# Kernel tuning notes

Hardware: AMD Instinct MI355X
Metric: run time of the kernel (lower is better)

## Reference

```python
import jax, jax.numpy as jnp
from jax import lax
import numpy as np

OUT_CH = 16      # texture_features
INTER = 32       # texture_features_intermediate
TEXDIM = 1024    # texture_dimensions
IN_SIZE = 76


def _leaky(x):
    return jnp.where(x >= 0, x, 0.02 * x)


def grid_sample_bilinear_border(tex, grid):
    """torch.nn.functional.grid_sample, mode='bilinear', padding_mode='border',
    align_corners=False.  tex: (N,C,H,W); grid: (N,Ho,Wo,2) with (x,y) in [-1,1].
    N == 1 here; vectorized over H,W via fancy indexing."""
    N, C, H, W = tex.shape
    x, y = grid[..., 0], grid[..., 1]
    # unnormalize (align_corners=False)
    ix = ((x + 1.0) * W - 1.0) * 0.5
    iy = ((y + 1.0) * H - 1.0) * 0.5
    # border padding: clamp continuous coords
    ix = jnp.clip(ix, 0.0, W - 1.0)
    iy = jnp.clip(iy, 0.0, H - 1.0)
    x0 = jnp.floor(ix); y0 = jnp.floor(iy)
    wx = ix - x0; wy = iy - y0
    x0i = jnp.clip(x0, 0, W - 1).astype(jnp.int32)
    x1i = jnp.clip(x0 + 1, 0, W - 1).astype(jnp.int32)
    y0i = jnp.clip(y0, 0, H - 1).astype(jnp.int32)
    y1i = jnp.clip(y0 + 1, 0, H - 1).astype(jnp.int32)
    t = tex[0]  # (C,H,W)
    v00 = t[:, y0i[0], x0i[0]]  # (C,Ho,Wo)
    v01 = t[:, y0i[0], x1i[0]]
    v10 = t[:, y1i[0], x0i[0]]
    v11 = t[:, y1i[0], x1i[0]]
    wx = wx[0][None]; wy = wy[0][None]  # (1,Ho,Wo) broadcast over C
    out = (v00 * (1 - wx) * (1 - wy) + v01 * wx * (1 - wy)
           + v10 * (1 - wx) * wy + v11 * wx * wy)
    return out[None]  # (1,C,Ho,Wo)


def setup_inputs() -> dict:
    key = jax.random.key(0)
    ks = jax.random.split(key, 11)
    expressions = jax.random.normal(ks[0], (1, IN_SIZE), jnp.float32)
    audio_features = jax.random.normal(ks[1], (1, 16), jnp.float32)
    uv_inputs = jax.random.uniform(ks[2], (1, 2, 1024, 1024), jnp.float32, -1.0, 1.0)
    data = jax.random.normal(ks[3], (1, INTER, TEXDIM, TEXDIM), jnp.float32)
    def lin(kw, kb, fo, fi):
        s = 1.0 / np.sqrt(fi).astype(np.float32)
        return (jax.random.uniform(kw, (fo, fi), jnp.float32, -s, s),
                jax.random.uniform(kb, (fo,), jnp.float32, -s, s))
    W1, b1 = lin(ks[4], ks[5], 128, IN_SIZE)
    W2, b2 = lin(ks[6], ks[7], 64, 128)
    W3, b3 = lin(ks[8], ks[9], OUT_CH * 4 * 4 * INTER, 64)
    return {"expressions": expressions, "audio_features": audio_features,
            "uv_inputs": uv_inputs, "data": data,
            "W1": W1, "b1": b1, "W2": W2, "b2": b2, "W3": W3, "b3": b3}


def reference(expressions, audio_features, uv_inputs, data, W1, b1, W2, b2, W3, b3):
    # tiny MLP -> dynamic 4x4 conv filter
    h = expressions.reshape(1, 1, -1)
    h = _leaky(h @ W1.T + b1)
    h = _leaky(h @ W2.T + b2)
    f = jnp.tanh(h @ W3.T + b3)
    conv_filter = f.reshape(OUT_CH, INTER, 4, 4)
    # conv2d(data, filter, stride=1, padding=2) -> (1, OUT_CH, D+1, D+1)
    tex_eval = lax.conv_general_dilated(
        data, conv_filter, window_strides=(1, 1), padding=((2, 2), (2, 2)),
        dimension_numbers=("NCHW", "OIHW", "NCHW"))
    # grid: stack x (chan 0) and y (chan 1) along last dim
    grid = jnp.stack([uv_inputs[:, 0], uv_inputs[:, 1]], axis=3)  # (1,Ho,Wo,2)
    return grid_sample_bilinear_border(tex_eval, grid)
```

## Files before the change

### kernel.cpp

```cpp
#include <hip/hip_runtime.h>
#include <math.h>

#define NPX   1048576
#define TD    1025
#define PW    35
#define PH    11
#define DPAD  1028
#define ROWB  65792
#define DP_OFF 67289152

typedef _Float16 half8 __attribute__((ext_vector_type(8)));
typedef _Float16 half4 __attribute__((ext_vector_type(4)));
typedef float    f32x4 __attribute__((ext_vector_type(4)));

__device__ __forceinline__ void load_lds16(const void* g, void* lds) {
    __builtin_amdgcn_global_load_lds(
        (const __attribute__((address_space(1))) void*)g,
        (__attribute__((address_space(3))) void*)lds, 16, 0, 0);
}

__global__ __launch_bounds__(256) void mlp_kernel(
    const float* __restrict__ expr,
    const float* __restrict__ W1, const float* __restrict__ b1,
    const float* __restrict__ W2, const float* __restrict__ b2,
    const float* __restrict__ W3, const float* __restrict__ b3,
    _Float16* __restrict__ ffrag_g)
{
    __shared__ float sx[76];
    __shared__ float sh1[128];
    __shared__ float sh2[64];
    int t = threadIdx.x;
    if (t < 76) sx[t] = expr[t];
    __syncthreads();
    if (t < 128) {
        float a = b1[t];
        const float* w = W1 + t * 76;
        #pragma unroll 4
        for (int i = 0; i < 76; ++i) a += sx[i] * w[i];
        sh1[t] = a >= 0.f ? a : 0.02f * a;
    }
    __syncthreads();
    if (t < 64) {
        float a = b2[t];
        const float* w = W2 + t * 128;
        #pragma unroll 4
        for (int i = 0; i < 128; ++i) a += sh1[i] * w[i];
        sh2[t] = a >= 0.f ? a : 0.02f * a;
    }
    __syncthreads();
    int o = blockIdx.x * 256 + t;
    float a = b3[o];
    const float* w = W3 + o * 64;
    #pragma unroll 4
    for (int i = 0; i < 64; ++i) a += sh2[i] * w[i];
    a = tanhf(a);
    int oc = o >> 9;
    int ic = (o >> 4) & 31;
    int kk = o & 15;
    ffrag_g[(size_t)(kk * 64 + (ic >> 3) * 16 + oc) * 8 + (ic & 7)] = (_Float16)a;
}

__global__ __launch_bounds__(256) void repack_kernel(
    const float* __restrict__ data, _Float16* __restrict__ Dp)
{
    __shared__ _Float16 s[256 * 32];
    int tid = threadIdx.x;
    int Y = blockIdx.y;
    int X = blockIdx.x * 256 + tid;
    int y = Y - 2, x = X - 2;
    bool ok = ((unsigned)y < 1024u) && ((unsigned)x < 1024u);
    const float* dp = data + ((size_t)y << 10) + x;

    float v[32];
    #pragma unroll
    for (int j = 0; j < 32; ++j) v[j] = 0.f;
    if (ok) {
        #pragma unroll
        for (int j = 0; j < 32; ++j) v[j] = __builtin_nontemporal_load(&dp[(size_t)j * NPX]);
    }
    #pragma unroll
    for (int g = 0; g < 4; ++g) {
        half8 h;
        #pragma unroll
        for (int j = 0; j < 8; ++j) h[j] = (_Float16)v[g * 8 + j];
        int chunk = tid * 4 + g;
        int sw = chunk ^ ((chunk >> 3) & 7);
        *(half8*)((char*)s + sw * 16) = h;
    }
    __syncthreads();
    char* rowbase = (char*)Dp + (size_t)Y * ROWB + blockIdx.x * 16384;
    int lim = ROWB - blockIdx.x * 16384;
    #pragma unroll
    for (int i = 0; i < 4; ++i) {
        int off = tid * 16 + i * 4096;
        if (off < lim) {
            int chunk = tid + i * 256;
            int sw = chunk ^ ((chunk >> 3) & 7);
            *(uint4*)(rowbase + off) = *(uint4*)((char*)s + sw * 16);
        }
    }
}

__global__ __launch_bounds__(256, 6) void conv_mfma_kernel(
    const _Float16* __restrict__ Dp,
    const _Float16* __restrict__ ffrag_g,
    _Float16* __restrict__ tex)
{
    __shared__ __attribute__((aligned(128))) _Float16 sp[PH * PW * 32];

    int tid = threadIdx.x;
    int l = tid & 63, w = tid >> 6;
    int ox0 = blockIdx.x * 32;
    int oy0 = blockIdx.y * 8;

    half8 bfrag[16];
    #pragma unroll
    for (int kk = 0; kk < 16; ++kk)
        bfrag[kk] = *(const half8*)&ffrag_g[kk * 512 + l * 8];

    int lsw = l ^ ((l >> 3) & 7);
    for (int r = w; r < PH; r += 4) {
        int gy = min(oy0 + r, DPAD - 1);
        const char* grow = (const char*)Dp + (size_t)gy * ROWB;
        _Float16* lrow = sp + r * (PW * 32);
        #pragma unroll
        for (int c = 0; c < 3; ++c) {
            int off = ox0 * 64 + c * 1024 + lsw * 16;
            off = min(off, ROWB - 16);
            if (c < 2 || l < 12)
                load_lds16(grow + off, (char*)lrow + c * 1024);
        }
    }
    __syncthreads();

    int lane15 = l & 15;
    int q = l >> 4;

    int u = lane15 * 4 + q;
    int sv[4];
    #pragma unroll
    for (int kx = 0; kx < 4; ++kx) {
        int vch = kx * 4 + u;
        sv[kx] = (vch ^ ((vch >> 3) & 7)) * 16;
    }

    f32x4 acc[4];
    #pragma unroll
    for (int t = 0; t < 4; ++t) acc[t] = (f32x4){0.f, 0.f, 0.f, 0.f};

    #pragma unroll 4
    for (int kk = 0; kk < 16; ++kk) {
        int ky = kk >> 2, kx = kk & 3;
        #pragma unroll
        for (int t = 0; t < 4; ++t) {
            const char* ap = (const char*)sp
                + (w * 2 + (t >> 1) + ky) * (PW * 64)
                + (t & 1) * 1024 + sv[kx];
            half8 af = *(const half8*)ap;
            acc[t] = __builtin_amdgcn_mfma_f32_16x16x32_f16(bfrag[kk], af, acc[t], 0, 0, 0);
        }
    }

    #pragma unroll
    for (int t = 0; t < 4; ++t) {
        int oy = oy0 + w * 2 + (t >> 1);
        int px = ox0 + (t & 1) * 16 + lane15;
        if (oy > 1024 || px > 1024) continue;
        half4 hv;
        #pragma unroll
        for (int r = 0; r < 4; ++r) hv[r] = (_Float16)acc[t][r];
        size_t base = ((size_t)oy * TD + px) * 32;
        *(half4*)&tex[base + q * 4] = hv;
        if (px > 0)
            *(half4*)&tex[base - 16 + q * 4] = hv;
        if (px == 1024)
            *(half4*)&tex[base + 16 + q * 4] = hv;
    }
}

__global__ __launch_bounds__(256, 6) void sample_kernel(
    const float* __restrict__ uv,
    const _Float16* __restrict__ tex,
    float* __restrict__ out)
{
    int p = blockIdx.x * 256 + threadIdx.x;
    float x = __builtin_nontemporal_load(&uv[p]);
    float y = __builtin_nontemporal_load(&uv[NPX + p]);
    float ix = fminf(fmaxf(((x + 1.f) * 1025.f - 1.f) * 0.5f, 0.f), 1024.f);
    float iy = fminf(fmaxf(((y + 1.f) * 1025.f - 1.f) * 0.5f, 0.f), 1024.f);
    float fx0 = floorf(ix), fy0 = floorf(iy);
    float wx = ix - fx0, wy = iy - fy0;
    int x0 = (int)fx0, y0 = (int)fy0;
    int y1 = min(y0 + 1, 1024);

    const half8* r0 = (const half8*)(tex + ((size_t)y0 * TD + x0) * 32);
    const half8* r1 = (const half8*)(tex + ((size_t)y1 * TD + x0) * 32);

    half8 v0 = r0[0], v1 = r0[1];
    half8 v2 = r0[2], v3 = r0[3];
    half8 v4 = r1[0], v5 = r1[1];
    half8 v6 = r1[2], v7 = r1[3];

    float w00 = (1.f - wx) * (1.f - wy);
    float w01 = wx * (1.f - wy);
    float w10 = (1.f - wx) * wy;
    float w11 = wx * wy;

    #pragma unroll
    for (int c = 0; c < 8; ++c) {
        float r0v = (float)v0[c] * w00 + (float)v2[c] * w01
                  + (float)v4[c] * w10 + (float)v6[c] * w11;
        float r1v = (float)v1[c] * w00 + (float)v3[c] * w01
                  + (float)v5[c] * w10 + (float)v7[c] * w11;
        __builtin_nontemporal_store(r0v, &out[(size_t)c * NPX + p]);
        __builtin_nontemporal_store(r1v, &out[(size_t)(c + 8) * NPX + p]);
    }
}

extern "C" void kernel_launch(void* const* d_in, const int* in_sizes, int n_in,
                              void* d_out, int out_size, void* d_ws, size_t ws_size,
                              hipStream_t stream) {
    const float* expr = (const float*)d_in[0];
    const float* uv   = (const float*)d_in[2];
    const float* data = (const float*)d_in[3];
    const float* W1   = (const float*)d_in[4];
    const float* b1   = (const float*)d_in[5];
    const float* W2   = (const float*)d_in[6];
    const float* b2   = (const float*)d_in[7];
    const float* W3   = (const float*)d_in[8];
    const float* b3   = (const float*)d_in[9];
    float* out = (float*)d_out;

    _Float16* ffrag_g  = (_Float16*)d_ws;
    _Float16* tex2     = (_Float16*)((char*)d_ws + 49152);
    _Float16* Dp       = (_Float16*)((char*)d_ws + DP_OFF);

    mlp_kernel<<<32, 256, 0, stream>>>(expr, W1, b1, W2, b2, W3, b3, ffrag_g);
    repack_kernel<<<dim3(5, DPAD), 256, 0, stream>>>(data, Dp);
    conv_mfma_kernel<<<dim3(33, 129), 256, 0, stream>>>(Dp, ffrag_g, tex2);
    sample_kernel<<<NPX / 256, 256, 0, stream>>>(uv, tex2, out);
}
```

Before: 396.9 us.

## Store conv texture without duplicated neighbor; sample four corners; two pixels per thread

The conv output texture stops storing each pixel's right neighbour alongside it, which halves the texture footprint and cuts the conv kernel's write traffic. The sampler now gathers four separate 32-byte corners instead of two 64-byte pairs. Each sampler thread also handles two pixels to raise memory-level parallelism, with lower occupancy as the cost. The workspace offset shrinks to match the smaller texture. This adds more scattered gather requests in the sampler in exchange for fewer bytes written.

```diff
diff --git a/kernel.cpp b/kernel.cpp
--- a/kernel.cpp
+++ b/kernel.cpp
@@ -7,7 +7,7 @@
 #define PH    11
 #define DPAD  1028
 #define ROWB  65792
-#define DP_OFF 67289152
+#define DP_OFF 33673216
 
 typedef _Float16 half8 __attribute__((ext_vector_type(8)));
 typedef _Float16 half4 __attribute__((ext_vector_type(4)));
@@ -169,51 +169,78 @@
         half4 hv;
         #pragma unroll
         for (int r = 0; r < 4; ++r) hv[r] = (_Float16)acc[t][r];
-        size_t base = ((size_t)oy * TD + px) * 32;
-        *(half4*)&tex[base + q * 4] = hv;
-        if (px > 0)
-            *(half4*)&tex[base - 16 + q * 4] = hv;
-        if (px == 1024)
-            *(half4*)&tex[base + 16 + q * 4] = hv;
-    }
-}
-
-__global__ __launch_bounds__(256, 6) void sample_kernel(
+        *(half4*)&tex[((size_t)oy * TD + px) * 16 + q * 4] = hv;
+    }
+}
+
+__global__ __launch_bounds__(256, 4) void sample_kernel(
     const float* __restrict__ uv,
     const _Float16* __restrict__ tex,
     float* __restrict__ out)
 {
-    int p = blockIdx.x * 256 + threadIdx.x;
-    float x = __builtin_nontemporal_load(&uv[p]);
-    float y = __builtin_nontemporal_load(&uv[NPX + p]);
-    float ix = fminf(fmaxf(((x + 1.f) * 1025.f - 1.f) * 0.5f, 0.f), 1024.f);
-    float iy = fminf(fmaxf(((y + 1.f) * 1025.f - 1.f) * 0.5f, 0.f), 1024.f);
-    float fx0 = floorf(ix), fy0 = floorf(iy);
-    float wx = ix - fx0, wy = iy - fy0;
-    int x0 = (int)fx0, y0 = (int)fy0;
-    int y1 = min(y0 + 1, 1024);
-
-    const half8* r0 = (const half8*)(tex + ((size_t)y0 * TD + x0) * 32);
-    const half8* r1 = (const half8*)(tex + ((size_t)y1 * TD + x0) * 32);
-
-    half8 v0 = r0[0], v1 = r0[1];
-    half8 v2 = r0[2], v3 = r0[3];
-    half8 v4 = r1[0], v5 = r1[1];
-    half8 v6 = r1[2], v7 = r1[3];
-
-    float w00 = (1.f - wx) * (1.f - wy);
-    float w01 = wx * (1.f - wy);
-    float w10 = (1.f - wx) * wy;
-    float w11 = wx * wy;
+    int pa = blockIdx.x * 512 + threadIdx.x;
+    int pb = pa + 256;
+
+    float xa = __builtin_nontemporal_load(&uv[pa]);
+    float ya = __builtin_nontemporal_load(&uv[NPX + pa]);
+    float xb = __builtin_nontemporal_load(&uv[pb]);
+    float yb = __builtin_nontemporal_load(&uv[NPX + pb]);
+
+    float ixa = fminf(fmaxf(((xa + 1.f) * 1025.f - 1.f) * 0.5f, 0.f), 1024.f);
+    float iya = fminf(fmaxf(((ya + 1.f) * 1025.f - 1.f) * 0.5f, 0.f), 1024.f);
+    float ixb = fminf(fmaxf(((xb + 1.f) * 1025.f - 1.f) * 0.5f, 0.f), 1024.f);
+    float iyb = fminf(fmaxf(((yb + 1.f) * 1025.f - 1.f) * 0.5f, 0.f), 1024.f);
+
+    float fxa = floorf(ixa), fya = floorf(iya);
+    float fxb = floorf(ixb), fyb = floorf(iyb);
+    float wxa = ixa - fxa, wya = iya - fya;
+    float wxb = ixb - fxb, wyb = iyb - fyb;
+    int x0a = (int)fxa, y0a = (int)fya;
+    int x0b = (int)fxb, y0b = (int)fyb;
+    int x1a = min(x0a + 1, 1024), y1a = min(y0a + 1, 1024);
+    int x1b = min(x0b + 1, 1024), y1b = min(y0b + 1, 1024);
+
+    const half8* a00 = (const half8*)(tex + ((size_t)y0a * TD + x0a) * 16);
+    const half8* a01 = (const half8*)(tex + ((size_t)y0a * TD + x1a) * 16);
+    const half8* a10 = (const half8*)(tex + ((size_t)y1a * TD + x0a) * 16);
+    const half8* a11 = (const half8*)(tex + ((size_t)y1a * TD + x1a) * 16);
+    const half8* b00 = (const half8*)(tex + ((size_t)y0b * TD + x0b) * 16);
+    const half8* b01 = (const half8*)(tex + ((size_t)y0b * TD + x1b) * 16);
+    const half8* b10 = (const half8*)(tex + ((size_t)y1b * TD + x0b) * 16);
+    const half8* b11 = (const half8*)(tex + ((size_t)y1b * TD + x1b) * 16);
+
+    half8 va0 = a00[0], va1 = a00[1];
+    half8 va2 = a01[0], va3 = a01[1];
+    half8 va4 = a10[0], va5 = a10[1];
+    half8 va6 = a11[0], va7 = a11[1];
+    half8 vb0 = b00[0], vb1 = b00[1];
+    half8 vb2 = b01[0], vb3 = b01[1];
+    half8 vb4 = b10[0], vb5 = b10[1];
+    half8 vb6 = b11[0], vb7 = b11[1];
+
+    float wa00 = (1.f - wxa) * (1.f - wya);
+    float wa01 = wxa * (1.f - wya);
+    float wa10 = (1.f - wxa) * wya;
+    float wa11 = wxa * wya;
+    float wb00 = (1.f - wxb) * (1.f - wyb);
+    float wb01 = wxb * (1.f - wyb);
+    float wb10 = (1.f - wxb) * wyb;
+    float wb11 = wxb * wyb;
 
     #pragma unroll
     for (int c = 0; c < 8; ++c) {
-        float r0v = (float)v0[c] * w00 + (float)v2[c] * w01
-                  + (float)v4[c] * w10 + (float)v6[c] * w11;
-        float r1v = (float)v1[c] * w00 + (float)v3[c] * w01
-                  + (float)v5[c] * w10 + (float)v7[c] * w11;
-        __builtin_nontemporal_store(r0v, &out[(size_t)c * NPX + p]);
-        __builtin_nontemporal_store(r1v, &out[(size_t)(c + 8) * NPX + p]);
+        float ra0 = (float)va0[c] * wa00 + (float)va2[c] * wa01
+                  + (float)va4[c] * wa10 + (float)va6[c] * wa11;
+        float ra1 = (float)va1[c] * wa00 + (float)va3[c] * wa01
+                  + (float)va5[c] * wa10 + (float)va7[c] * wa11;
+        float rb0 = (float)vb0[c] * wb00 + (float)vb2[c] * wb01
+                  + (float)vb4[c] * wb10 + (float)vb6[c] * wb11;
+        float rb1 = (float)vb1[c] * wb00 + (float)vb3[c] * wb01
+                  + (float)vb5[c] * wb10 + (float)vb7[c] * wb11;
+        __builtin_nontemporal_store(ra0, &out[(size_t)c * NPX + pa]);
+        __builtin_nontemporal_store(ra1, &out[(size_t)(c + 8) * NPX + pa]);
+        __builtin_nontemporal_store(rb0, &out[(size_t)c * NPX + pb]);
+        __builtin_nontemporal_store(rb1, &out[(size_t)(c + 8) * NPX + pb]);
     }
 }
 
@@ -232,11 +259,11 @@
     float* out = (float*)d_out;
 
     _Float16* ffrag_g  = (_Float16*)d_ws;
-    _Float16* tex2     = (_Float16*)((char*)d_ws + 49152);
+    _Float16* tex      = (_Float16*)((char*)d_ws + 49152);
     _Float16* Dp       = (_Float16*)((char*)d_ws + DP_OFF);
 
     mlp_kernel<<<32, 256, 0, stream>>>(expr, W1, b1, W2, b2, W3, b3, ffrag_g);
     repack_kernel<<<dim3(5, DPAD), 256, 0, stream>>>(data, Dp);
-    conv_mfma_kernel<<<dim3(33, 129), 256, 0, stream>>>(Dp, ffrag_g, tex2);
-    sample_kernel<<<NPX / 256, 256, 0, stream>>>(uv, tex2, out);
-}
+    conv_mfma_kernel<<<dim3(33, 129), 256, 0, stream>>>(Dp, ffrag_g, tex);
+    sample_kernel<<<NPX / 512, 256, 0, stream>>>(uv, tex, out);
+}
```

Result: slower. 405.5 us (+2.2%).
